# Performance work log

Hardware: AMD Instinct MI355X
Metric: run time of the kernel (lower is better)

The kernel has to match this reference:

```python
import jax, jax.numpy as jnp
import numpy as np

L, B, D, H = 128, 4, 768, 300
NT, NR = 7, 12  # ner tags, relation types
EPS = 1e-5


def _cummax(v):
    # torch: cumsum(softmax(v, -1), -1)
    return jnp.cumsum(jax.nn.softmax(v, axis=-1), axis=-1)


def _layernorm(v, g, b):
    mu = jnp.mean(v, axis=-1, keepdims=True)
    var = jnp.var(v, axis=-1, keepdims=True)
    return (v - mu) * jax.lax.rsqrt(var + EPS) * g + b


def setup_inputs() -> dict:
    key = jax.random.key(0)
    ks = jax.random.split(key, 24)
    s = lambda fan_in: 1.0 / np.sqrt(fan_in)
    u = lambda k, shape, sc: jax.random.uniform(k, shape, jnp.float32, -sc, sc)
    inp = {
        "x": jax.random.normal(ks[0], (L, B, D), jnp.float32),
        "mask": jnp.ones((L, B), jnp.float32),
        # PFN_Unit
        "W_ih": u(ks[1], (5 * H, D), s(D)), "b_ih": u(ks[2], (5 * H,), s(D)),
        "W_hh": u(ks[3], (5 * H, H), s(H)), "b_hh": u(ks[4], (5 * H,), s(H)),
        "W_tr": u(ks[5], (H, 3 * H), s(3 * H)), "b_tr": u(ks[6], (H,), s(3 * H)),
        # NERUnit
        "n_W": u(ks[7], (H, 2 * H), s(2 * H)), "n_b": u(ks[8], (H,), s(2 * H)),
        "ner_hW": u(ks[9], (H, 3 * H), s(3 * H)), "ner_hb": u(ks[10], (H,), s(3 * H)),
        "ner_g": jnp.ones((H,), jnp.float32), "ner_beta": jnp.zeros((H,), jnp.float32),
        "ner_tW": u(ks[11], (NT, H), s(H)), "ner_tb": u(ks[12], (NT,), s(H)),
        # ReUnit
        "r_W": u(ks[13], (H, 2 * H), s(2 * H)), "r_b": u(ks[14], (H,), s(2 * H)),
        "re_hW": u(ks[15], (H, 3 * H), s(3 * H)), "re_hb": u(ks[16], (H,), s(3 * H)),
        "re_g": jnp.ones((H,), jnp.float32), "re_beta": jnp.zeros((H,), jnp.float32),
        "re_tW": u(ks[17], (NR, H), s(H)), "re_tb": u(ks[18], (NR,), s(H)),
    }
    return inp


def _encoder(x, W_ih, b_ih, W_hh, b_hh, W_tr, b_tr):
    pre = jnp.einsum('lbd,gd->lbg', x, W_ih) + b_ih  # precompute input transform [L,B,5H]

    def step(carry, gx):
        h, c_in = carry
        gates = gx + h @ W_hh.T + b_hh
        c, eg_cin, rg_cin, eg_c, rg_c = jnp.split(gates, 5, axis=1)
        eg_cin, rg_cin = 1.0 - _cummax(eg_cin), _cummax(rg_cin)
        eg_c, rg_c = 1.0 - _cummax(eg_c), _cummax(rg_c)
        c = jnp.tanh(c)
        ov_c = rg_c * eg_c
        up_c, dn_c = rg_c - ov_c, eg_c - ov_c
        ov_i = rg_cin * eg_cin
        up_i, dn_i = rg_cin - ov_i, eg_cin - ov_i
        share = ov_i * c_in + ov_c * c
        c_re = up_i * c_in + up_c * c + share
        c_ner = dn_i * c_in + dn_c * c + share
        c_out = jnp.concatenate([c_re, c_ner, share], axis=-1) @ W_tr.T + b_tr
        h_out = jnp.tanh(c_out)
        return (h_out, c_out), (jnp.tanh(c_ner), jnp.tanh(c_re), jnp.tanh(share))

    h0 = jnp.zeros((x.shape[1], W_hh.shape[1]), x.dtype)
    _, (h_ner, h_re, h_share) = jax.lax.scan(step, (h0, h0), pre)
    return h_ner, h_re, h_share  # each [L,B,H]


def _pair_unit(h_task, h_share, mask, gW, gb, hW, hb, ln_g, ln_b, tW, tb, diag):
    length = h_task.shape[0]
    # global feature: tanh(Linear(cat(share, task))), max over time
    h_glob = jnp.tanh(jnp.concatenate([h_share, h_task], axis=-1) @ gW.T + gb)  # [L,B,H]
    g = jnp.max(h_glob, axis=0)  # [B,H]
    # pairwise feature [L,L,B,3H] = cat(start, end, global)
    st = jnp.broadcast_to(h_task[:, None], (length, length) + h_task.shape[1:])
    en = jnp.broadcast_to(h_task[None, :], (length, length) + h_task.shape[1:])
    gb4 = jnp.broadcast_to(g, (length, length) + g.shape)
    feat = jnp.concatenate([st, en, gb4], axis=-1)
    out = _layernorm(feat @ hW.T + hb, ln_g, ln_b)
    out = jax.nn.elu(out)  # eval mode: dropout is identity
    out = jax.nn.sigmoid(out @ tW.T + tb)  # [L,L,B,T]
    # mask
    m = mask[:, None, :] * mask[None, :, :]  # [L,L,B]
    if diag:
        m = m * jnp.triu(jnp.ones((length, length), out.dtype))[:, :, None]
    return out * m[..., None]


def reference(x, mask, W_ih, b_ih, W_hh, b_hh, W_tr, b_tr,
              n_W, n_b, ner_hW, ner_hb, ner_g, ner_beta, ner_tW, ner_tb,
              r_W, r_b, re_hW, re_hb, re_g, re_beta, re_tW, re_tb):
    h_ner, h_re, h_share = _encoder(x, W_ih, b_ih, W_hh, b_hh, W_tr, b_tr)
    ner = _pair_unit(h_ner, h_share, mask, n_W, n_b, ner_hW, ner_hb,
                     ner_g, ner_beta, ner_tW, ner_tb, diag=True)
    re = _pair_unit(h_re, h_share, mask, r_W, r_b, re_hW, re_hb,
                    re_g, re_beta, re_tW, re_tb, diag=False)
    return ner, re
```

## Files before the change

kernel.cpp:

```cpp
#include <hip/hip_runtime.h>

#define LLEN 128
#define BB 4
#define DD 768
#define HH 300
#define G5 1500
#define H3 900
#define NTT 7
#define NRR 12
#define NCHB 10
#define RPB 150
#define OPB 30

#define C_WIH  0
#define C_X    1152000
#define C_WHH2 1545216
#define C_WTR2 1995216
#define F_BIH  2265216
#define F_BTR  2266720
#define F_PRE  2267040
#define F_HG0  (F_PRE)
#define F_HG1  (F_PRE+153600)
#define F_A0   (F_PRE+307200)
#define F_E0   (F_PRE+460800)
#define F_GF0  (F_PRE+616832)
#define F_GF1  (F_PRE+618048)
#define F_HNER (F_PRE+768000)
#define F_HRE  (F_HNER+153600)
#define F_HSH  (F_HRE+153600)
#define F_A1   0
#define F_E1   153600
#define F_AUX  (F_HSH+153600)
#define AUXB   2432
#define AUX_FL 9728
#define WS_NEED_BYTES ((size_t)(F_AUX+10752)*4)

typedef unsigned short u16;
typedef unsigned int u32;

__device__ __forceinline__ float bf2f(u16 u) {
  union { u32 i; float f; } v; v.i = ((u32)u) << 16; return v.f;
}
__device__ __forceinline__ u16 f2bf(float f) {
  union { float f; u32 i; } v; v.f = f;
  u32 r = v.i + 0x7fffu + ((v.i >> 16) & 1u);
  return (u16)(r >> 16);
}
__device__ __forceinline__ float ldin(const void* p, int i, bool f32) {
  return f32 ? ((const float*)p)[i] : bf2f(((const u16*)p)[i]);
}
__device__ __forceinline__ bool is32(const void* mk) {
  return ((const u16*)mk)[0] == 0;
}
__device__ __forceinline__ float wsum(float x) {
  #pragma unroll
  for (int d = 1; d < 64; d <<= 1) x += __shfl_xor(x, d);
  return x;
}
__device__ __forceinline__ float aload(const float* p) {
  int v = __hip_atomic_load((const int*)p, __ATOMIC_RELAXED, __HIP_MEMORY_SCOPE_AGENT);
  union { int i; float f; } u; u.i = v; return u.f;
}
__device__ __forceinline__ void astore(float* p, float v) {
  union { float f; int i; } u; u.f = v;
  __hip_atomic_store((int*)p, u.i, __ATOMIC_RELAXED, __HIP_MEMORY_SCOPE_AGENT);
}
__device__ __forceinline__ void gbar(int* flag, int tid, int target) {
  __syncthreads();
  if (tid == 0) {
    __builtin_amdgcn_s_waitcnt(0);
    __hip_atomic_fetch_add(flag, 1, __ATOMIC_RELAXED, __HIP_MEMORY_SCOPE_AGENT);
    while (__hip_atomic_load(flag, __ATOMIC_RELAXED, __HIP_MEMORY_SCOPE_AGENT) < target)
      __builtin_amdgcn_s_sleep(1);
  }
  __syncthreads();
}

__global__ void k_canon(const void* xo, const void* mk, const void* Wih, const void* bih,
                        const void* Whh, const void* bhh, const void* Wtr, const void* btr,
                        float* ws) {
  bool f32 = is32(mk);
  int piece = blockIdx.y;
  int i = blockIdx.x * 256 + threadIdx.x;
  switch (piece) {
    case 0: if (!f32 && i < 1152000) ws[C_WIH + i] = ldin(Wih, i, f32); break;
    case 1: if (!f32 && i < 393216)  ws[C_X + i]   = ldin(xo, i, f32);  break;
    case 2: if (i < 225000) {
      int k2 = i / G5, out = i - k2 * G5;
      float2 v;
      v.x = ldin(Whh, out * HH + 2 * k2, f32);
      v.y = ldin(Whh, out * HH + 2 * k2 + 1, f32);
      ((float2*)(ws + C_WHH2))[i] = v;
    } break;
    case 3: if (i < 135000) {
      int k2 = i / HH, out = i - k2 * HH;
      float2 v;
      v.x = ldin(Wtr, out * H3 + 2 * k2, f32);
      v.y = ldin(Wtr, out * H3 + 2 * k2 + 1, f32);
      ((float2*)(ws + C_WTR2))[i] = v;
    } break;
    case 4: {
      if (i < 1504) ws[F_BIH + i] = (i < G5) ? ldin(bih, i, f32) + ldin(bhh, i, f32) : 0.f;
      else if (i < 1824) { int j = i - 1504; ws[F_BTR + j] = (j < HH) ? ldin(btr, j, f32) : 0.f; }
    } break;
    case 5: if (i < 1024) ((int*)(ws + F_AUX + AUX_FL))[i] = 0; break;
  }
}

__global__ void k_pre2(const void* xo, const void* Wo, const void* mk,
                       const float* cX, const float* cW, const float* biasf, float* pre) {
  bool f32 = is32(mk);
  const float* X = f32 ? (const float*)xo : cX;
  const float* W = f32 ? (const float*)Wo : cW;
  __shared__ __align__(16) float xl[8 * DD];
  int tid = threadIdx.x;
  int lb0 = (blockIdx.x >> 1) * 8;
  int half = blockIdx.x & 1;
  for (int e = tid; e < 8 * DD; e += 256) xl[e] = X[(size_t)lb0 * DD + e];
  __syncthreads();
  for (int j = half * 750 + tid; j < half * 750 + 750; j += 256) {
    const float4* w = (const float4*)(W + (size_t)j * DD);
    float acc[8] = {0.f, 0.f, 0.f, 0.f, 0.f, 0.f, 0.f, 0.f};
    #pragma unroll 2
    for (int k = 0; k < DD / 4; ++k) {
      float4 u = w[k];
      #pragma unroll
      for (int r = 0; r < 8; ++r) {
        const float4 p = *(const float4*)(xl + r * DD + k * 4);
        acc[r] += u.x * p.x + u.y * p.y + u.z * p.z + u.w * p.w;
      }
    }
    float bias = biasf[j];
    #pragma unroll
    for (int r = 0; r < 8; ++r) pre[(size_t)(lb0 + r) * G5 + j] = acc[r] + bias;
  }
}

__global__ void __launch_bounds__(512, 2) k_scan4(const float* pre, const float2* W2h, const float2* W2t,
                                                  const float* btrf, float* hner, float* hre, float* hsh,
                                                  float* aux) {
  __shared__ __align__(16) float h_l[304];
  __shared__ __align__(16) float ci_l[304];
  __shared__ __align__(16) float ga_l[1504];
  __shared__ __align__(16) float cat_l[904];
  __shared__ __align__(16) float ps[512];
  __shared__ float exv[160];
  __shared__ float pp[40];
  __shared__ float sums_l[8];
  int b = blockIdx.x / NCHB, ch = blockIdx.x % NCHB;
  int s = ch >> 1;
  int r0 = ch * RPB;
  int tid = threadIdx.x;
  float* gb   = aux + b * AUXB;
  float* cb   = gb + 1504;
  float* hb   = gb + 1808;
  float* sums = gb + 2112;
  int* flags = (int*)(aux + AUX_FL) + b * 256;
  for (int i = tid; i < 304; i += 512) { h_l[i] = 0.f; ci_l[i] = 0.f; }
  __syncthreads();
  int j = tid / RPB, r = tid - j * RPB;
  int o2 = tid % OPB, jj = tid / OPB;
  int kb = j * 100;

  float2 wh[50];
  if (tid < 450) {
    const float2* wp = W2h + (size_t)(j * 50) * G5 + (r0 + r);
    #pragma unroll
    for (int kk = 0; kk < 50; ++kk) wh[kk] = wp[(size_t)kk * G5];
  }
  float2 wt[29];
  int k2b = jj * 29;
  int k2e = (k2b + 29 < 450) ? (k2b + 29) : 450;
  int nk2 = k2e - k2b;
  if (tid < 480) {
    const float2* wp = W2t + (size_t)k2b * HH + (ch * OPB + o2);
    #pragma unroll
    for (int q = 0; q < 29; ++q) if (q < nk2) wt[q] = wp[(size_t)q * HH];
  }

  for (int t = 0; t < LLEN; ++t) {
    if (t > 0) {
      for (int i = tid; i < HH; i += 512) { h_l[i] = aload(hb + i); ci_l[i] = aload(cb + i); }
      __syncthreads();
    }
    if (tid < 450) {
      float acc = (j == 0) ? pre[((size_t)t * BB + b) * G5 + r0 + r] : 0.f;
      if (t > 0) {
        #pragma unroll
        for (int kk = 0; kk < 50; ++kk)
          acc += wh[kk].x * h_l[kb + 2 * kk] + wh[kk].y * h_l[kb + 2 * kk + 1];
      }
      ps[tid] = acc;
    }
    __syncthreads();
    if (tid < RPB) {
      float g = ps[tid] + ps[RPB + tid] + ps[2 * RPB + tid];
      if (s == 0) astore(gb + r0 + tid, tanhf(g));
      else exv[tid] = __expf(g);
    }
    __syncthreads();
    if (s > 0) {
      if (tid < 30) {
        int base = tid * 5;
        pp[tid] = ((exv[base] + exv[base+1]) + (exv[base+2] + exv[base+3])) + exv[base+4];
      }
      __syncthreads();
      if (tid == 0) {
        float run = 0.f;
        for (int i = 0; i < 30; ++i) { float tv = pp[i]; pp[i] = run; run += tv; }
        astore(sums + (ch - 2), run);
      }
      __syncthreads();
      if (tid < 30) {
        int base = tid * 5;
        float run = pp[tid];
        run += exv[base];     astore(gb + r0 + base,     run);
        run += exv[base + 1]; astore(gb + r0 + base + 1, run);
        run += exv[base + 2]; astore(gb + r0 + base + 2, run);
        run += exv[base + 3]; astore(gb + r0 + base + 3, run);
        run += exv[base + 4]; astore(gb + r0 + base + 4, run);
      }
    }
    gbar(flags + 2 * t, tid, NCHB);
    for (int i = tid; i < G5; i += 512) ga_l[i] = aload(gb + i);
    if (tid < 8) sums_l[tid] = aload(sums + tid);
    __syncthreads();
    if (tid < HH) {
      float c = ga_l[tid];
      float v[4];
      #pragma unroll
      for (int s1 = 0; s1 < 4; ++s1) {
        float raw = ga_l[(s1 + 1) * HH + tid];
        float off = (tid >= RPB) ? sums_l[2 * s1] : 0.f;
        float S = sums_l[2 * s1] + sums_l[2 * s1 + 1];
        v[s1] = (raw + off) / S;
      }
      float eg_cin = 1.f - v[0], rg_cin = v[1], eg_c = 1.f - v[2], rg_c = v[3];
      float ci = (t > 0) ? ci_l[tid] : 0.f;
      float ov_c = rg_c * eg_c;
      float up_c = rg_c - ov_c, dn_c = eg_c - ov_c;
      float ov_i = rg_cin * eg_cin;
      float up_i = rg_cin - ov_i, dn_i = eg_cin - ov_i;
      float share = ov_i * ci + ov_c * c;
      float c_re  = up_i * ci + up_c * c + share;
      float c_ner = dn_i * ci + dn_c * c + share;
      cat_l[tid] = c_re; cat_l[HH + tid] = c_ner; cat_l[2 * HH + tid] = share;
      int sb = ch * OPB;
      if (tid >= sb && tid < sb + OPB) {
        size_t ob = ((size_t)t * BB + b) * HH + tid;
        hner[ob] = tanhf(c_ner); hre[ob] = tanhf(c_re); hsh[ob] = tanhf(share);
      }
    }
    __syncthreads();
    if (tid < 480) {
      float acc = 0.f;
      #pragma unroll
      for (int q = 0; q < 29; ++q)
        if (q < nk2) acc += wt[q].x * cat_l[2 * (k2b + q)] + wt[q].y * cat_l[2 * (k2b + q) + 1];
      ps[tid] = acc;
    }
    __syncthreads();
    if (tid < OPB) {
      float co = btrf[ch * OPB + tid];
      #pragma unroll
      for (int q = 0; q < 16; ++q) co += ps[q * OPB + tid];
      astore(cb + ch * OPB + tid, co);
      astore(hb + ch * OPB + tid, tanhf(co));
    }
    gbar(flags + 2 * t + 1, tid, NCHB);
  }
}

__global__ void k_glob3(const float* hsh, const float* hner, const float* hre,
                        const void* nW, const void* nb, const void* rW, const void* rb,
                        const void* mk, float* hg0, float* hg1) {
  bool f32 = is32(mk);
  int task = blockIdx.x >> 7;
  int lb0 = (blockIdx.x & 127) * 4;
  const float* tsk = task ? hre : hner;
  const void* gWo = task ? rW : nW;
  const void* gbo = task ? rb : nb;
  float* hg = task ? hg1 : hg0;
  __shared__ __align__(16) float catl[2400];
  int tid = threadIdx.x;
  for (int e = tid; e < 2400; e += 320) {
    int rr = e / 600, c = e - rr * 600;
    catl[e] = (c < HH) ? hsh[(size_t)(lb0 + rr) * HH + c] : tsk[(size_t)(lb0 + rr) * HH + (c - HH)];
  }
  __syncthreads();
  if (tid < HH) {
    float bias = ldin(gbo, tid, f32);
    float acc[4] = {bias, bias, bias, bias};
    if (f32) {
      const float4* row = (const float4*)((const float*)gWo + (size_t)tid * 600);
      #pragma unroll 2
      for (int k = 0; k < 150; ++k) {
        float4 u = row[k];
        #pragma unroll
        for (int rr = 0; rr < 4; ++rr) {
          const float4 cv = *(const float4*)(catl + rr * 600 + 4 * k);
          acc[rr] += u.x * cv.x + u.y * cv.y + u.z * cv.z + u.w * cv.w;
        }
      }
    } else {
      for (int k = 0; k < 600; ++k) {
        float w = ldin(gWo, tid * 600 + k, f32);
        #pragma unroll
        for (int rr = 0; rr < 4; ++rr) acc[rr] += w * catl[rr * 600 + k];
      }
    }
    #pragma unroll
    for (int rr = 0; rr < 4; ++rr) hg[(size_t)(lb0 + rr) * HH + tid] = tanhf(acc[rr]);
  }
}

__global__ void k_feat2(const float* hner, const float* hre,
                        const void* nhW, const void* nhb, const void* rhW, const void* rhb,
                        const void* mk, float* A0, float* E0, float* A1, float* E1) {
  bool f32 = is32(mk);
  int task = blockIdx.x >> 7;
  int lb0 = (blockIdx.x & 127) * 4;
  const float* tsk = task ? hre : hner;
  const void* hWo = task ? rhW : nhW;
  const void* hbo = task ? rhb : nhb;
  float* A = task ? A1 : A0;
  float* E = task ? E1 : E0;
  __shared__ __align__(16) float tl[1200];
  int tid = threadIdx.x;
  for (int e = tid; e < 1200; e += 320) {
    int rr = e / 300, c = e - rr * 300;
    tl[e] = tsk[(size_t)(lb0 + rr) * HH + c];
  }
  __syncthreads();
  if (tid < HH) {
    float bias = ldin(hbo, tid, f32);
    float a[4] = {bias, bias, bias, bias};
    float ev[4] = {0.f, 0.f, 0.f, 0.f};
    if (f32) {
      const float4* r1 = (const float4*)((const float*)hWo + (size_t)tid * H3);
      const float4* r2 = (const float4*)((const float*)hWo + (size_t)tid * H3 + HH);
      #pragma unroll 2
      for (int k = 0; k < 75; ++k) {
        float4 u = r1[k], w2 = r2[k];
        #pragma unroll
        for (int rr = 0; rr < 4; ++rr) {
          const float4 tv = *(const float4*)(tl + rr * 300 + 4 * k);
          a[rr]  += u.x * tv.x + u.y * tv.y + u.z * tv.z + u.w * tv.w;
          ev[rr] += w2.x * tv.x + w2.y * tv.y + w2.z * tv.z + w2.w * tv.w;
        }
      }
    } else {
      for (int k = 0; k < HH; ++k) {
        float w1 = ldin(hWo, tid * H3 + k, f32);
        float w2 = ldin(hWo, tid * H3 + HH + k, f32);
        #pragma unroll
        for (int rr = 0; rr < 4; ++rr) {
          a[rr] += w1 * tl[rr * 300 + k];
          ev[rr] += w2 * tl[rr * 300 + k];
        }
      }
    }
    #pragma unroll
    for (int rr = 0; rr < 4; ++rr) {
      A[(size_t)(lb0 + rr) * HH + tid] = a[rr];
      E[(size_t)(lb0 + rr) * HH + tid] = ev[rr];
    }
  }
}

__global__ void k_gmf(const float* hg0, const float* hg1, const void* nhW, const void* rhW,
                      const void* mk, float* Gf0, float* Gf1) {
  bool f32 = is32(mk);
  int task = blockIdx.x >> 2, b = blockIdx.x & 3;
  const float* hg = task ? hg1 : hg0;
  const void* hWo = task ? rhW : nhW;
  float* Gf = task ? Gf1 : Gf0;
  __shared__ __align__(16) float gl[304];
  int tid = threadIdx.x;
  if (tid < HH) {
    float m = -1e30f;
    for (int l = 0; l < LLEN; ++l) m = fmaxf(m, hg[((size_t)l * BB + b) * HH + tid]);
    gl[tid] = m;
  }
  __syncthreads();
  if (tid < HH) {
    float acc = 0.f;
    if (f32) {
      const float4* row = (const float4*)((const float*)hWo + (size_t)tid * H3 + 600);
      #pragma unroll 5
      for (int k = 0; k < 75; ++k) {
        float4 u = row[k];
        const float4 gv = *(const float4*)(gl + 4 * k);
        acc += u.x * gv.x + u.y * gv.y + u.z * gv.z + u.w * gv.w;
      }
    } else {
      for (int k = 0; k < HH; ++k) acc += gl[k] * ldin(hWo, tid * H3 + 600 + k, f32);
    }
    Gf[b * HH + tid] = acc;
  }
}

__global__ void __launch_bounds__(256) k_pair6(const float* A0, const float* E0, const float* Gf0,
                                               const void* lg0, const void* lb0_, const void* tW0, const void* tb0,
                                               const float* A1, const float* E1, const float* Gf1,
                                               const void* lg1, const void* lb1_, const void* tW1, const void* tb1,
                                               const void* mk, void* outv) {
  __shared__ float lg_l[304], lb_l[304], tb_l[16];
  __shared__ float tw_l[3616];
  bool f32 = is32(mk);
  int tau = blockIdx.x >> 12;
  int bid = blockIdx.x & 4095;
  const float* A  = tau ? A1 : A0;
  const float* E  = tau ? E1 : E0;
  const float* Gf = tau ? Gf1 : Gf0;
  const void* lgo = tau ? lg1 : lg0;
  const void* lbo = tau ? lb1_ : lb0_;
  const void* tWo = tau ? tW1 : tW0;
  const void* tbo = tau ? tb1 : tb0;
  int T = tau ? NRR : NTT;
  int diag = tau ? 0 : 1;
  int Toff = tau ? 458752 : 0;
  int tid = threadIdx.x;
  for (int i2 = tid; i2 < HH; i2 += 256) { lg_l[i2] = ldin(lgo, i2, f32); lb_l[i2] = ldin(lbo, i2, f32); }
  for (int i2 = tid; i2 < T * HH; i2 += 256) tw_l[i2] = ldin(tWo, i2, f32);
  if (tid < T) tb_l[tid] = ldin(tbo, tid, f32);
  __syncthreads();
  int i = bid >> 5;
  int j0 = (bid & 31) << 2;
  int b = tid >> 6, ln = tid & 63;
  const float* ar = A  + (size_t)(i * BB + b) * HH;
  const float* gr = Gf + (size_t)b * HH;
  bool ok4 = ln < 44;
  float a0 = ar[ln]       + gr[ln];
  float a1 = ar[64 + ln]  + gr[64 + ln];
  float a2 = ar[128 + ln] + gr[128 + ln];
  float a3 = ar[192 + ln] + gr[192 + ln];
  float a4 = ok4 ? (ar[256 + ln] + gr[256 + ln]) : 0.f;
  float mi = ldin(mk, i * BB + b, f32);
  for (int dj = 0; dj < 4; ++dj) {
    int jx = j0 + dj;
    const float* er = E + (size_t)(jx * BB + b) * HH;
    float u0 = a0 + er[ln];
    float u1 = a1 + er[64 + ln];
    float u2 = a2 + er[128 + ln];
    float u3 = a3 + er[192 + ln];
    float u4 = ok4 ? (a4 + er[256 + ln]) : 0.f;
    float s1 = ((u0 + u1) + (u2 + u3)) + u4;
    float s2 = ((u0 * u0 + u1 * u1) + (u2 * u2 + u3 * u3)) + u4 * u4;
    #pragma unroll
    for (int d = 1; d < 64; d <<= 1) { s1 += __shfl_xor(s1, d); s2 += __shfl_xor(s2, d); }
    float mean = s1 * (1.f / 300.f);
    float var = s2 * (1.f / 300.f) - mean * mean;
    float rstd = rsqrtf(var + 1e-5f);
    {
      float y;
      y = (u0 - mean) * rstd * lg_l[ln]       + lb_l[ln];       u0 = (y > 0.f) ? y : __expf(y) - 1.f;
      y = (u1 - mean) * rstd * lg_l[64 + ln]  + lb_l[64 + ln];  u1 = (y > 0.f) ? y : __expf(y) - 1.f;
      y = (u2 - mean) * rstd * lg_l[128 + ln] + lb_l[128 + ln]; u2 = (y > 0.f) ? y : __expf(y) - 1.f;
      y = (u3 - mean) * rstd * lg_l[192 + ln] + lb_l[192 + ln]; u3 = (y > 0.f) ? y : __expf(y) - 1.f;
      if (ok4) {
        y = (u4 - mean) * rstd * lg_l[256 + ln] + lb_l[256 + ln];
        u4 = (y > 0.f) ? y : __expf(y) - 1.f;
      }
    }
    float m = mi * ldin(mk, jx * BB + b, f32);
    if (diag && jx < i) m = 0.f;
    size_t obase = (size_t)Toff + ((size_t)(i * LLEN + jx) * BB + b) * T;
    float mine = 0.f;
    for (int t = 0; t < T; ++t) {
      const float* twr = tw_l + t * HH;
      float s = u0 * twr[ln] + u1 * twr[64 + ln] + u2 * twr[128 + ln] + u3 * twr[192 + ln];
      if (ok4) s += u4 * twr[256 + ln];
      s = wsum(s);
      s += tb_l[t];
      float o = m / (1.f + __expf(-s));
      mine = (ln == t) ? o : mine;
    }
    if (ln < T) {
      if (f32) ((float*)outv)[obase + ln] = mine;
      else ((u16*)outv)[obase + ln] = f2bf(mine);
    }
  }
}

__global__ void k_sent(const void* mk, const void* xo, void* outv, int hostcode) {
  __shared__ int bad;
  if (threadIdx.x == 0) bad = 0;
  __syncthreads();
  bool f32 = is32(mk);
  for (int i = threadIdx.x; i < 4096; i += 256) {
    float v = ldin(xo, i, f32);
    if (!(v == v) || fabsf(v) > 1e6f) bad = 1;
  }
  __syncthreads();
  if (threadIdx.x == 0) {
    float code = (float)hostcode;
    if (bad) code = fmaxf(code, 88.f);
    if (code > 0.f) {
      if (f32) ((float*)outv)[0] = code;
      else ((u16*)outv)[0] = f2bf(code);
    }
  }
}

extern "C" void kernel_launch(void* const* d_in, const int* in_sizes, int n_in,
                              void* d_out, int out_size, void* d_ws, size_t ws_size,
                              hipStream_t stream) {
  const void* x    = d_in[0];
  const void* mask = d_in[1];
  const void* Wih  = d_in[2];
  const void* bih  = d_in[3];
  const void* Whh  = d_in[4];
  const void* bhh  = d_in[5];
  const void* Wtr  = d_in[6];
  const void* btr  = d_in[7];
  const void* nW   = d_in[8];
  const void* nb   = d_in[9];
  const void* nhW  = d_in[10];
  const void* nhb  = d_in[11];
  const void* ng   = d_in[12];
  const void* nbe  = d_in[13];
  const void* ntW  = d_in[14];
  const void* ntb  = d_in[15];
  const void* rW   = d_in[16];
  const void* rb   = d_in[17];
  const void* rhW  = d_in[18];
  const void* rhb  = d_in[19];
  const void* rg   = d_in[20];
  const void* rbe  = d_in[21];
  const void* rtW  = d_in[22];
  const void* rtb  = d_in[23];
  float* ws = (float*)d_ws;

  static const int exp_sz[24] = {393216, 512, 1152000, 1500, 450000, 1500, 270000, 300,
                                 180000, 300, 270000, 300, 300, 300, 2100, 7,
                                 180000, 300, 270000, 300, 300, 300, 3600, 12};
  int hostcode = 0;
  if (n_in != 24) hostcode = 890;
  else {
    for (int ii = 0; ii < 24; ++ii)
      if (in_sizes[ii] != exp_sz[ii]) { hostcode = 900 + ii; break; }
  }
  if (hostcode == 0 && out_size != 1245184) hostcode = 880;
  if (hostcode == 0 && ws_size < WS_NEED_BYTES) hostcode = 1099;

  dim3 gc(4500, 6);
  k_canon<<<gc, 256, 0, stream>>>(x, mask, Wih, bih, Whh, bhh, Wtr, btr, ws);
  k_pre2<<<128, 256, 0, stream>>>(x, Wih, mask, ws + C_X, ws + C_WIH, ws + F_BIH, ws + F_PRE);
  k_scan4<<<40, 512, 0, stream>>>(ws + F_PRE, (const float2*)(ws + C_WHH2), (const float2*)(ws + C_WTR2),
                                  ws + F_BIH + 1504 - 1504 + (F_BTR - F_BIH), ws + F_HNER, ws + F_HRE, ws + F_HSH, ws + F_AUX);
  k_glob3<<<256, 320, 0, stream>>>(ws + F_HSH, ws + F_HNER, ws + F_HRE,
                                   nW, nb, rW, rb, mask, ws + F_HG0, ws + F_HG1);
  k_feat2<<<256, 320, 0, stream>>>(ws + F_HNER, ws + F_HRE, nhW, nhb, rhW, rhb, mask,
                                   ws + F_A0, ws + F_E0, ws + F_A1, ws + F_E1);
  k_gmf<<<8, 320, 0, stream>>>(ws + F_HG0, ws + F_HG1, nhW, rhW, mask, ws + F_GF0, ws + F_GF1);
  k_pair6<<<8192, 256, 0, stream>>>(ws + F_A0, ws + F_E0, ws + F_GF0, ng, nbe, ntW, ntb,
                                    ws + F_A1, ws + F_E1, ws + F_GF1, rg, rbe, rtW, rtb,
                                    mask, d_out);
  k_sent<<<1, 256, 0, stream>>>(mask, x, d_out, hostcode);
}
```

Before: 1.546 ms.

## Place scan blocks per XCD and sync through L2 instead of device-scope atomics

```diff
diff --git a/kernel.cpp b/kernel.cpp
--- a/kernel.cpp
+++ b/kernel.cpp
@@ -33,10 +33,11 @@
 #define F_AUX  (F_HSH+153600)
 #define AUXB   2432
 #define AUX_FL 9728
-#define WS_NEED_BYTES ((size_t)(F_AUX+10752)*4)
+#define WS_NEED_BYTES ((size_t)(F_AUX+11776)*4)
 
 typedef unsigned short u16;
 typedef unsigned int u32;
+typedef float f4 __attribute__((ext_vector_type(4)));
 
 __device__ __forceinline__ float bf2f(u16 u) {
   union { u32 i; float f; } v; v.i = ((u32)u) << 16; return v.f;
@@ -74,6 +75,42 @@
       __builtin_amdgcn_s_sleep(1);
   }
   __syncthreads();
+}
+
+__device__ __forceinline__ f4 ld4_l2(const f4* p) {
+  f4 v;
+  asm volatile("global_load_dwordx4 %0, %1, off sc0\n\ts_waitcnt vmcnt(0)"
+               : "=v"(v) : "v"(p) : "memory");
+  return v;
+}
+__device__ __forceinline__ float ld1_l2(const float* p) {
+  float v;
+  asm volatile("global_load_dword %0, %1, off sc0\n\ts_waitcnt vmcnt(0)"
+               : "=v"(v) : "v"(p) : "memory");
+  return v;
+}
+__device__ __forceinline__ int ldi_l2(const int* p) {
+  int v;
+  asm volatile("global_load_dword %0, %1, off sc0\n\ts_waitcnt vmcnt(0)"
+               : "=v"(v) : "v"(p) : "memory");
+  return v;
+}
+__device__ __forceinline__ void gbarL2(int* flag, int tid, int target) {
+  __builtin_amdgcn_s_waitcnt(0);
+  __syncthreads();
+  if (tid == 0) {
+    __builtin_amdgcn_s_waitcnt(0);
+    __hip_atomic_fetch_add(flag, 1, __ATOMIC_RELAXED, __HIP_MEMORY_SCOPE_WORKGROUP);
+    int it = 0;
+    while (ldi_l2(flag) < target) {
+      __builtin_amdgcn_s_sleep(1);
+      if (++it > 100000) break;
+    }
+  }
+  __syncthreads();
+}
+__device__ __forceinline__ void exst(float* p, float v, int mode) {
+  if (mode) *p = v; else astore(p, v);
 }
 
 __global__ void k_canon(const void* xo, const void* mk, const void* Wih, const void* bih,
@@ -103,7 +140,7 @@
       if (i < 1504) ws[F_BIH + i] = (i < G5) ? ldin(bih, i, f32) + ldin(bhh, i, f32) : 0.f;
       else if (i < 1824) { int j = i - 1504; ws[F_BTR + j] = (j < HH) ? ldin(btr, j, f32) : 0.f; }
     } break;
-    case 5: if (i < 1024) ((int*)(ws + F_AUX + AUX_FL))[i] = 0; break;
+    case 5: if (i < 11776) ws[F_AUX + i] = 0.f; break;
   }
 }
 
@@ -136,7 +173,7 @@
   }
 }
 
-__global__ void __launch_bounds__(512, 2) k_scan4(const float* pre, const float2* W2h, const float2* W2t,
+__global__ void __launch_bounds__(512, 2) k_scan6(const float* pre, const float2* W2h, const float2* W2t,
                                                   const float* btrf, float* hner, float* hre, float* hsh,
                                                   float* aux) {
   __shared__ __align__(16) float h_l[304];
@@ -144,20 +181,73 @@
   __shared__ __align__(16) float ga_l[1504];
   __shared__ __align__(16) float cat_l[904];
   __shared__ __align__(16) float ps[512];
+  __shared__ __align__(16) float sums_l[8];
   __shared__ float exv[160];
   __shared__ float pp[40];
-  __shared__ float sums_l[8];
-  int b = blockIdx.x / NCHB, ch = blockIdx.x % NCHB;
+  __shared__ int s_bc;
+  __shared__ int s_mode;
+  int tid = threadIdx.x;
+  int* ibase = (int*)(aux + AUX_FL);
+  if (tid == 0) {
+    int* cl = ibase + 1024;
+    unsigned xcd;
+    asm volatile("s_getreg_b32 %0, hwreg(HW_REG_XCC_ID)" : "=s"(xcd));
+    xcd &= 7u;
+    int rank = __hip_atomic_fetch_add(cl + xcd, 1, __ATOMIC_RELAXED, __HIP_MEMORY_SCOPE_AGENT);
+    __hip_atomic_fetch_add(cl + 8, 1, __ATOMIC_RELAXED, __HIP_MEMORY_SCOPE_AGENT);
+    int it = 0;
+    while (__hip_atomic_load(cl + 8, __ATOMIC_RELAXED, __HIP_MEMORY_SCOPE_AGENT) < (int)gridDim.x) {
+      __builtin_amdgcn_s_sleep(2);
+      if (++it > 200000) break;
+    }
+    int base = 0;
+    for (unsigned x = 0; x < xcd; ++x)
+      base += __hip_atomic_load(cl + x, __ATOMIC_RELAXED, __HIP_MEMORY_SCOPE_AGENT) / NCHB;
+    int cnt = __hip_atomic_load(cl + xcd, __ATOMIC_RELAXED, __HIP_MEMORY_SCOPE_AGENT);
+    int slot = base + rank / NCHB;
+    s_bc = (rank < (cnt / NCHB) * NCHB && slot < BB) ? (slot * 16 + rank % NCHB) : -1;
+  }
+  __syncthreads();
+  int bc = s_bc;
+  if (bc < 0) return;
+  int b = bc >> 4, ch = bc & 15;
   int s = ch >> 1;
   int r0 = ch * RPB;
-  int tid = threadIdx.x;
   float* gb   = aux + b * AUXB;
   float* cb   = gb + 1504;
   float* hb   = gb + 1808;
   float* sums = gb + 2112;
-  int* flags = (int*)(aux + AUX_FL) + b * 256;
+  int* flags = ibase + b * 256;
+
+  {
+    int* atf = ibase + 1088 + b * 32;
+    float* tst = gb + 2176;
+    int* seflag = (int*)(gb + 2208);
+    if (ch == 0 && tid == 0) tst[0] = 1.0f;
+    gbar(atf + 0, tid, NCHB);
+    if (tid == 0) { float w1 = ld1_l2(tst); (void)w1; }
+    gbar(atf + 1, tid, NCHB);
+    if (ch == 0 && tid == 0) {
+      tst[0] = 2.0f;
+      __builtin_amdgcn_s_waitcnt(0);
+    }
+    if (ch == 1 && tid == 0)
+      __hip_atomic_fetch_add(seflag, 1, __ATOMIC_RELAXED, __HIP_MEMORY_SCOPE_WORKGROUP);
+    gbar(atf + 2, tid, NCHB);
+    if (tid == 0) {
+      float w2 = ld1_l2(tst);
+      int fv = ldi_l2(seflag);
+      if (w2 != 2.0f || fv != 1)
+        __hip_atomic_fetch_or(atf + 4, 1, __ATOMIC_RELAXED, __HIP_MEMORY_SCOPE_AGENT);
+    }
+    gbar(atf + 3, tid, NCHB);
+    if (tid == 0)
+      s_mode = (__hip_atomic_load(atf + 4, __ATOMIC_RELAXED, __HIP_MEMORY_SCOPE_AGENT) == 0) ? 1 : 0;
+    __syncthreads();
+  }
+  int mode = s_mode;
+
   for (int i = tid; i < 304; i += 512) { h_l[i] = 0.f; ci_l[i] = 0.f; }
-  __syncthreads();
   int j = tid / RPB, r = tid - j * RPB;
   int o2 = tid % OPB, jj = tid / OPB;
   int kb = j * 100;
@@ -177,14 +267,22 @@
     #pragma unroll
     for (int q = 0; q < 29; ++q) if (q < nk2) wt[q] = wp[(size_t)q * HH];
   }
+  __syncthreads();
 
   for (int t = 0; t < LLEN; ++t) {
+    float pv = 0.f;
+    if (j == 0 && tid < 450) pv = pre[((size_t)t * BB + b) * G5 + r0 + r];
     if (t > 0) {
-      for (int i = tid; i < HH; i += 512) { h_l[i] = aload(hb + i); ci_l[i] = aload(cb + i); }
+      if (mode) {
+        if (tid < 75)       { f4 v = ld4_l2((const f4*)hb + tid); *(f4*)(h_l + 4 * tid) = v; }
+        else if (tid < 150) { int q = tid - 75; f4 v = ld4_l2((const f4*)cb + q); *(f4*)(ci_l + 4 * q) = v; }
+      } else {
+        for (int i = tid; i < HH; i += 512) { h_l[i] = aload(hb + i); ci_l[i] = aload(cb + i); }
+      }
       __syncthreads();
     }
     if (tid < 450) {
-      float acc = (j == 0) ? pre[((size_t)t * BB + b) * G5 + r0 + r] : 0.f;
+      float acc = pv;
       if (t > 0) {
         #pragma unroll
         for (int kk = 0; kk < 50; ++kk)
@@ -195,35 +293,40 @@
     __syncthreads();
     if (tid < RPB) {
       float g = ps[tid] + ps[RPB + tid] + ps[2 * RPB + tid];
-      if (s == 0) astore(gb + r0 + tid, tanhf(g));
+      if (s == 0) exst(gb + r0 + tid, tanhf(g), mode);
       else exv[tid] = __expf(g);
     }
     __syncthreads();
     if (s > 0) {
       if (tid < 30) {
-        int base = tid * 5;
-        pp[tid] = ((exv[base] + exv[base+1]) + (exv[base+2] + exv[base+3])) + exv[base+4];
+        int base2 = tid * 5;
+        pp[tid] = ((exv[base2] + exv[base2+1]) + (exv[base2+2] + exv[base2+3])) + exv[base2+4];
       }
       __syncthreads();
       if (tid == 0) {
         float run = 0.f;
         for (int i = 0; i < 30; ++i) { float tv = pp[i]; pp[i] = run; run += tv; }
-        astore(sums + (ch - 2), run);
+        exst(sums + (ch - 2), run, mode);
       }
       __syncthreads();
       if (tid < 30) {
-        int base = tid * 5;
+        int base2 = tid * 5;
         float run = pp[tid];
-        run += exv[base];     astore(gb + r0 + base,     run);
-        run += exv[base + 1]; astore(gb + r0 + base + 1, run);
-        run += exv[base + 2]; astore(gb + r0 + base + 2, run);
-        run += exv[base + 3]; astore(gb + r0 + base + 3, run);
-        run += exv[base + 4]; astore(gb + r0 + base + 4, run);
-      }
-    }
-    gbar(flags + 2 * t, tid, NCHB);
-    for (int i = tid; i < G5; i += 512) ga_l[i] = aload(gb + i);
-    if (tid < 8) sums_l[tid] = aload(sums + tid);
+        run += exv[base2];     exst(gb + r0 + base2,     run, mode);
+        run += exv[base2 + 1]; exst(gb + r0 + base2 + 1, run, mode);
+        run += exv[base2 + 2]; exst(gb + r0 + base2 + 2, run, mode);
+        run += exv[base2 + 3]; exst(gb + r0 + base2 + 3, run, mode);
+        run += exv[base2 + 4]; exst(gb + r0 + base2 + 4, run, mode);
+      }
+    }
+    if (mode) gbarL2(flags + 2 * t, tid, NCHB); else gbar(flags + 2 * t, tid, NCHB);
+    if (mode) {
+      if (tid < 375)      { f4 v = ld4_l2((const f4*)gb + tid); *(f4*)(ga_l + 4 * tid) = v; }
+      else if (tid < 377) { int q = tid - 375; f4 v = ld4_l2((const f4*)sums + q); *(f4*)(sums_l + 4 * q) = v; }
+    } else {
+      for (int i = tid; i < G5; i += 512) ga_l[i] = aload(gb + i);
+      if (tid < 8) sums_l[tid] = aload(sums + tid);
+    }
     __syncthreads();
     if (tid < HH) {
       float c = ga_l[tid];
@@ -264,10 +367,10 @@
       float co = btrf[ch * OPB + tid];
       #pragma unroll
       for (int q = 0; q < 16; ++q) co += ps[q * OPB + tid];
-      astore(cb + ch * OPB + tid, co);
-      astore(hb + ch * OPB + tid, tanhf(co));
-    }
-    gbar(flags + 2 * t + 1, tid, NCHB);
+      exst(cb + ch * OPB + tid, co, mode);
+      exst(hb + ch * OPB + tid, tanhf(co), mode);
+    }
+    if (mode) gbarL2(flags + 2 * t + 1, tid, NCHB); else gbar(flags + 2 * t + 1, tid, NCHB);
   }
 }
 
@@ -547,8 +650,8 @@
   dim3 gc(4500, 6);
   k_canon<<<gc, 256, 0, stream>>>(x, mask, Wih, bih, Whh, bhh, Wtr, btr, ws);
   k_pre2<<<128, 256, 0, stream>>>(x, Wih, mask, ws + C_X, ws + C_WIH, ws + F_BIH, ws + F_PRE);
-  k_scan4<<<40, 512, 0, stream>>>(ws + F_PRE, (const float2*)(ws + C_WHH2), (const float2*)(ws + C_WTR2),
-                                  ws + F_BIH + 1504 - 1504 + (F_BTR - F_BIH), ws + F_HNER, ws + F_HRE, ws + F_HSH, ws + F_AUX);
+  k_scan6<<<256, 512, 0, stream>>>(ws + F_PRE, (const float2*)(ws + C_WHH2), (const float2*)(ws + C_WTR2),
+                                   ws + F_BTR, ws + F_HNER, ws + F_HRE, ws + F_HSH, ws + F_AUX);
   k_glob3<<<256, 320, 0, stream>>>(ws + F_HSH, ws + F_HNER, ws + F_HRE,
                                    nW, nb, rW, rb, mask, ws + F_HG0, ws + F_HG1);
   k_feat2<<<256, 320, 0, stream>>>(ws + F_HNER, ws + F_HRE, nhW, nhb, rhW, rhb, mask,
```

Measured after the change: 1.527 ms. Within noise of the previous version (-1.2%).
